# Kernel optimization log

Hardware: AMD Instinct MI355X
Metric: run time of the kernel (lower is better)

## Reference

```python
import jax, jax.numpy as jnp
import numpy as np

NEG_SLOPE = 0.2
EPS = 1e-16


def _gat_conv(x, edge_index, W, att_src, att_dst, bias):
    """PyG-style GATConv: linear -> per-edge attention -> segment softmax over dst -> scatter-sum.
    x: [N, Fin], W: [Fin, H*F], att_src/att_dst: [H, F], bias: [H*F].
    Adds self-loops (PyG default)."""
    N = x.shape[0]
    H, F = att_src.shape
    h = (x @ W).reshape(N, H, F)                       # [N, H, F]
    loops = jnp.arange(N, dtype=edge_index.dtype)
    src = jnp.concatenate([edge_index[0], loops])      # [E+N]
    dst = jnp.concatenate([edge_index[1], loops])
    a_s = jnp.sum(h * att_src[None], axis=-1)          # [N, H]
    a_d = jnp.sum(h * att_dst[None], axis=-1)          # [N, H]
    e = a_s[src] + a_d[dst]                            # [E+N, H]
    e = jnp.where(e > 0, e, NEG_SLOPE * e)             # leaky_relu
    m = jax.ops.segment_max(e, dst, num_segments=N)    # stable segment softmax
    ex = jnp.exp(e - m[dst])
    s = jax.ops.segment_sum(ex, dst, num_segments=N)
    alpha = ex / (s[dst] + EPS)                        # [E+N, H]
    msg = h[src] * alpha[..., None]                    # [E+N, H, F]
    out = jax.ops.segment_sum(msg, dst, num_segments=N)  # [N, H, F]
    return out.reshape(N, H * F) + bias


def setup_inputs() -> dict:
    key = jax.random.key(0)
    ks = jax.random.split(key, 12)
    N, E, Q = 200000, 6400000, 1000000
    return {
        "x": jax.random.normal(ks[0], (N, 1), jnp.float32),
        "edge_index": jax.random.randint(ks[1], (2, E), 0, N, jnp.int64),
        "src": jax.random.randint(ks[2], (Q,), 0, N, jnp.int64),
        "dst": jax.random.randint(ks[3], (Q,), 0, N, jnp.int64),
        "W1": jax.random.normal(ks[4], (1, 8), jnp.float32) * 0.5,
        "att_src1": jax.random.normal(ks[5], (2, 4), jnp.float32) * 0.5,
        "att_dst1": jax.random.normal(ks[6], (2, 4), jnp.float32) * 0.5,
        "b1": jnp.zeros((8,), jnp.float32),
        "W2": jax.random.normal(ks[7], (8, 8), jnp.float32) * 0.35,
        "att_src2": jax.random.normal(ks[8], (2, 4), jnp.float32) * 0.5,
        "att_dst2": jax.random.normal(ks[9], (2, 4), jnp.float32) * 0.5,
        "b2": jnp.zeros((8,), jnp.float32),
        "Wl": jax.random.normal(ks[10], (16, 2), jnp.float32) * 0.25,
        "bl": jnp.zeros((2,), jnp.float32),
    }


def reference(x, edge_index, src, dst, W1, att_src1, att_dst1, b1,
              W2, att_src2, att_dst2, b2, Wl, bl):
    h = _gat_conv(x, edge_index, W1, att_src1, att_dst1, b1)   # [N, 8]
    h = _gat_conv(h, edge_index, W2, att_src2, att_dst2, b2)   # [N, 8]
    y = jnp.concatenate([h[src], h[dst]], axis=-1)             # [Q, 16]
    return y @ Wl + bl                                         # [Q, 2]
```

## Files before the change

kernel.cpp:

```cpp
#include <hip/hip_runtime.h>
#include <hip/hip_fp16.h>

#define NEG_SLOPE 0.2f
#define GAT_EPS 1e-16f

#define BSHIFT 9
#define BSIZE 512
#define NBPAD 512
#define CAP_BKT 17664

#define K3_T 512
#define K3_VPT 16
#define K3_TILE (K3_T * K3_VPT)

#define CAP_BUILD 18432

#define LPD 16

typedef _Float16 half8 __attribute__((ext_vector_type(8)));

static __device__ __forceinline__ float leaky(float v) {
    return v > 0.0f ? v : NEG_SLOPE * v;
}


__global__ __launch_bounds__(K3_T) void bin_scatter_kernel(
        const int* __restrict__ src, const int* __restrict__ dst, int E, int NB,
        int* __restrict__ bcursor, unsigned int* __restrict__ binned) {
    extern __shared__ unsigned long long sbuf[];
    __shared__ int cnt[NBPAD];
    __shared__ int lstart[NBPAD];
    __shared__ int gbase[NBPAD];
    const int tid = threadIdx.x;
    const int t0 = blockIdx.x * K3_TILE;
    const int base = t0 + tid * K3_VPT;

    cnt[tid] = 0;
    __syncthreads();

    int b[K3_VPT];
    unsigned int v[K3_VPT];
    #pragma unroll
    for (int g = 0; g < K3_VPT / 4; ++g) {
        int off = base + g * 4;
        if (off < E) {
            int4 s4 = *(const int4*)(src + off);
            int4 d4 = *(const int4*)(dst + off);
            int ss[4] = {s4.x, s4.y, s4.z, s4.w};
            int dd[4] = {d4.x, d4.y, d4.z, d4.w};
            #pragma unroll
            for (int j = 0; j < 4; ++j) {
                int k = g * 4 + j;
                b[k] = dd[j] >> BSHIFT;
                v[k] = ((unsigned int)ss[j] << BSHIFT) | (unsigned int)(dd[j] & (BSIZE - 1));
                atomicAdd(&cnt[b[k]], 1);
            }
        } else {
            #pragma unroll
            for (int j = 0; j < 4; ++j) b[g * 4 + j] = -1;
        }
    }
    __syncthreads();

    int c = cnt[tid];
    lstart[tid] = c;
    __syncthreads();
    for (int ofs = 1; ofs < NBPAD; ofs <<= 1) {
        int t = (tid >= ofs) ? lstart[tid - ofs] : 0;
        __syncthreads();
        lstart[tid] += t;
        __syncthreads();
    }
    int excl = lstart[tid] - c;
    if (tid < NB) gbase[tid] = tid * CAP_BKT + (c ? atomicAdd(&bcursor[tid], c) : 0);
    __syncthreads();
    lstart[tid] = excl;
    cnt[tid] = 0;
    __syncthreads();

    #pragma unroll
    for (int k = 0; k < K3_VPT; ++k) {
        if (b[k] >= 0) {
            int r = atomicAdd(&cnt[b[k]], 1);
            int slot = lstart[b[k]] + r;
            sbuf[slot] = ((unsigned long long)(unsigned int)b[k] << 32) | v[k];
        }
    }
    __syncthreads();

    int nvalid = min(K3_TILE, E - t0);
    for (int j = tid; j < nvalid; j += K3_T) {
        unsigned long long p = sbuf[j];
        int bb = (int)(p >> 32);
        binned[gbase[bb] + (j - lstart[bb])] = (unsigned int)p;
    }
}


__global__ __launch_bounds__(BSIZE) void bucket_build_kernel(
        unsigned int* __restrict__ binned,
        const int* __restrict__ bcursor,
        int N,
        int2* __restrict__ rowrange) {
    extern __shared__ unsigned int sbuf32[];
    __shared__ int cnt[BSIZE];
    __shared__ int lstart[BSIZE];
    const int b = blockIdx.x;
    const int tid = threadIdx.x;
    const int e0 = b * CAP_BKT;
    const int nE = bcursor[b];
    const int n0 = b << BSHIFT;

    cnt[tid] = 0;
    __syncthreads();
    for (int i = tid; i < nE; i += BSIZE)
        atomicAdd(&cnt[binned[e0 + i] & (BSIZE - 1)], 1);
    __syncthreads();

    int c = cnt[tid];
    lstart[tid] = c;
    __syncthreads();
    for (int ofs = 1; ofs < BSIZE; ofs <<= 1) {
        int t = (tid >= ofs) ? lstart[tid - ofs] : 0;
        __syncthreads();
        lstart[tid] += t;
        __syncthreads();
    }
    int excl = lstart[tid] - c;
    __syncthreads();
    lstart[tid] = excl;
    cnt[tid] = 0;
    __syncthreads();

    int n = n0 + tid;
    if (n < N) rowrange[n] = make_int2(e0 + excl, e0 + excl + c);

    for (int i = tid; i < nE; i += BSIZE) {
        unsigned int v = binned[e0 + i];
        int dl = v & (BSIZE - 1);
        int r = atomicAdd(&cnt[dl], 1);
        int slot = lstart[dl] + r;
        if (slot < CAP_BUILD) sbuf32[slot] = v >> BSHIFT;
    }
    __syncthreads();

    int lim = min(nE, CAP_BUILD);
    for (int j = tid; j < lim; j += BSIZE)
        binned[e0 + j] = sbuf32[j];
}


__global__ void prep1_kernel(const float* __restrict__ x,
                             const float* __restrict__ W1,
                             const float* __restrict__ adw,
                             int N,
                             float2* __restrict__ adst,
                             half8* __restrict__ h16) {
    int n = blockIdx.x * blockDim.x + threadIdx.x;
    if (n >= N) return;
    float xv = x[n];
    float hv[8];
    #pragma unroll
    for (int j = 0; j < 8; ++j) hv[j] = xv * W1[j];
    float d0 = 0.f, d1 = 0.f;
    #pragma unroll
    for (int f = 0; f < 4; ++f) {
        d0 += hv[f] * adw[f];
        d1 += hv[4 + f] * adw[4 + f];
    }
    adst[n] = make_float2(d0, d1);
    half8 ho;
    #pragma unroll
    for (int j = 0; j < 8; ++j) ho[j] = (_Float16)hv[j];
    h16[n] = ho;
}


__global__ void prep2_kernel(const float* __restrict__ in,
                             const float* __restrict__ W2,
                             const float* __restrict__ adw,
                             int N,
                             float2* __restrict__ adst,
                             half8* __restrict__ h16) {
    int n = blockIdx.x * blockDim.x + threadIdx.x;
    if (n >= N) return;
    const float4* ip = (const float4*)(in + (size_t)n * 8);
    float4 i0 = ip[0], i1 = ip[1];
    float iv[8] = {i0.x, i0.y, i0.z, i0.w, i1.x, i1.y, i1.z, i1.w};
    float hv[8];
    #pragma unroll
    for (int j = 0; j < 8; ++j) {
        float acc = 0.f;
        #pragma unroll
        for (int k = 0; k < 8; ++k) acc += iv[k] * W2[k * 8 + j];
        hv[j] = acc;
    }
    float d0 = 0.f, d1 = 0.f;
    #pragma unroll
    for (int f = 0; f < 4; ++f) {
        d0 += hv[f] * adw[f];
        d1 += hv[4 + f] * adw[4 + f];
    }
    adst[n] = make_float2(d0, d1);
    half8 ho;
    #pragma unroll
    for (int j = 0; j < 8; ++j) ho[j] = (_Float16)hv[j];
    h16[n] = ho;
}


__global__ void gat_pass_kernel(const float2* __restrict__ adst,
                                const half8* __restrict__ h16,
                                const int2* __restrict__ rowrange,
                                const unsigned int* __restrict__ col,
                                const float* __restrict__ asw,
                                const float* __restrict__ bias,
                                int N,
                                float* __restrict__ out32,
                                half8* __restrict__ out16) {
    int t = blockIdx.x * blockDim.x + threadIdx.x;
    int n = t / LPD;
    int lane = t & (LPD - 1);
    if (n >= N) return;
    float w0 = asw[0], w1 = asw[1], w2 = asw[2], w3 = asw[3];
    float w4 = asw[4], w5 = asw[5], w6 = asw[6], w7 = asw[7];
    float2 ad = adst[n];
    float sum0 = 0.f, sum1 = 0.f;
    float acc[8] = {0.f, 0.f, 0.f, 0.f, 0.f, 0.f, 0.f, 0.f};
    if (lane == 0) {
        half8 hh = h16[n];
        float hs[8];
        #pragma unroll
        for (int k = 0; k < 8; ++k) hs[k] = (float)hh[k];
        float a0 = hs[0] * w0 + hs[1] * w1 + hs[2] * w2 + hs[3] * w3;
        float a1 = hs[4] * w4 + hs[5] * w5 + hs[6] * w6 + hs[7] * w7;
        float p0 = __expf(leaky(a0 + ad.x));
        float p1 = __expf(leaky(a1 + ad.y));
        sum0 = p0; sum1 = p1;
        #pragma unroll
        for (int k = 0; k < 4; ++k) { acc[k] = hs[k] * p0; acc[4 + k] = hs[4 + k] * p1; }
    }
    int2 rr = rowrange[n];
    int i = rr.x + lane;
    unsigned int s = (i < rr.y) ? __builtin_nontemporal_load(&col[i]) : 0u;
    while (i < rr.y) {
        int inext = i + LPD;
        unsigned int snext = (inext < rr.y) ? __builtin_nontemporal_load(&col[inext]) : 0u;
        half8 hh = h16[s];
        float hs[8];
        #pragma unroll
        for (int k = 0; k < 8; ++k) hs[k] = (float)hh[k];
        float a0 = hs[0] * w0 + hs[1] * w1 + hs[2] * w2 + hs[3] * w3;
        float a1 = hs[4] * w4 + hs[5] * w5 + hs[6] * w6 + hs[7] * w7;
        float q0 = __expf(leaky(a0 + ad.x));
        float q1 = __expf(leaky(a1 + ad.y));
        sum0 += q0; sum1 += q1;
        #pragma unroll
        for (int k = 0; k < 4; ++k) { acc[k] += hs[k] * q0; acc[4 + k] += hs[4 + k] * q1; }
        i = inext; s = snext;
    }
    #pragma unroll
    for (int ofs = 1; ofs < LPD; ofs <<= 1) {
        sum0 += __shfl_xor(sum0, ofs, LPD);
        sum1 += __shfl_xor(sum1, ofs, LPD);
        #pragma unroll
        for (int k = 0; k < 8; ++k) acc[k] += __shfl_xor(acc[k], ofs, LPD);
    }
    if (lane == 0) {
        float inv0 = 1.0f / (sum0 + GAT_EPS);
        float inv1 = 1.0f / (sum1 + GAT_EPS);
        float r[8];
        #pragma unroll
        for (int k = 0; k < 4; ++k) {
            r[k] = acc[k] * inv0 + bias[k];
            r[4 + k] = acc[4 + k] * inv1 + bias[4 + k];
        }
        if (out32) {
            float4* op = (float4*)(out32 + (size_t)n * 8);
            op[0] = make_float4(r[0], r[1], r[2], r[3]);
            op[1] = make_float4(r[4], r[5], r[6], r[7]);
        }
        if (out16) {
            half8 ho;
            #pragma unroll
            for (int k = 0; k < 8; ++k) ho[k] = (_Float16)r[k];
            out16[n] = ho;
        }
    }
}


__global__ void final_kernel(const half8* __restrict__ h2,
                             const int* __restrict__ srcq,
                             const int* __restrict__ dstq,
                             const float* __restrict__ Wl,
                             const float* __restrict__ bl,
                             int Q,
                             float* __restrict__ y) {
    int q = blockIdx.x * blockDim.x + threadIdx.x;
    if (q >= Q) return;
    int s = srcq[q];
    int d = dstq[q];
    half8 hs8 = h2[s];
    half8 hd8 = h2[d];
    float y0 = bl[0], y1 = bl[1];
    #pragma unroll
    for (int k = 0; k < 8; ++k) {
        float hv = (float)hs8[k];
        y0 += hv * Wl[k * 2 + 0];
        y1 += hv * Wl[k * 2 + 1];
    }
    #pragma unroll
    for (int k = 0; k < 8; ++k) {
        float hv = (float)hd8[k];
        y0 += hv * Wl[(8 + k) * 2 + 0];
        y1 += hv * Wl[(8 + k) * 2 + 1];
    }
    *(float2*)(y + (size_t)q * 2) = make_float2(y0, y1);
}


static inline size_t align_up(size_t v, size_t a) { return (v + a - 1) & ~(a - 1); }

extern "C" void kernel_launch(void* const* d_in, const int* in_sizes, int n_in,
                              void* d_out, int out_size, void* d_ws, size_t ws_size,
                              hipStream_t stream) {
    const float* x    = (const float*)d_in[0];
    const int*   ei   = (const int*)d_in[1];
    const int*   srcq = (const int*)d_in[2];
    const int*   dstq = (const int*)d_in[3];
    const float* W1   = (const float*)d_in[4];
    const float* as1  = (const float*)d_in[5];
    const float* ad1  = (const float*)d_in[6];
    const float* b1   = (const float*)d_in[7];
    const float* W2   = (const float*)d_in[8];
    const float* as2  = (const float*)d_in[9];
    const float* ad2  = (const float*)d_in[10];
    const float* b2   = (const float*)d_in[11];
    const float* Wl   = (const float*)d_in[12];
    const float* bl   = (const float*)d_in[13];

    const int N = in_sizes[0];
    const int E = in_sizes[1] / 2;
    const int Q = in_sizes[2];
    const int NB = (N + BSIZE - 1) >> BSHIFT;

    const int* esrc = ei;
    const int* edst = ei + E;

    char* w = (char*)d_ws;
    unsigned int* binned = (unsigned int*)w;  w += align_up((size_t)NB * CAP_BKT * 4, 256);
    int*    bcursor  = (int*)w;               w += align_up((size_t)NBPAD * 4, 256);
    int2*   rowrange = (int2*)w;              w += align_up((size_t)N * 8, 256);
    half8*  h16  = (half8*)w;                 w += align_up((size_t)N * 16, 256);
    float2* adst = (float2*)w;                w += align_up((size_t)N * 8, 256);
    float*  out1 = (float*)w;                 w += align_up((size_t)N * 8 * 4, 256);
    half8*  out2h = (half8*)w;

    const int BT = 256;
    int nodeBlocks = (N + BT - 1) / BT;
    int gatBlocks  = ((N * LPD) + BT - 1) / BT;
    int qBlocks    = (Q + BT - 1) / BT;
    int k3Blocks   = (E + K3_TILE - 1) / K3_TILE;

    hipMemsetAsync(bcursor, 0, (size_t)NBPAD * 4, stream);
    bin_scatter_kernel<<<k3Blocks, K3_T, (size_t)K3_TILE * 8, stream>>>(
        esrc, edst, E, NB, bcursor, binned);
    bucket_build_kernel<<<NB, BSIZE, (size_t)CAP_BUILD * 4, stream>>>(
        binned, bcursor, N, rowrange);

    prep1_kernel<<<nodeBlocks, BT, 0, stream>>>(x, W1, ad1, N, adst, h16);
    gat_pass_kernel<<<gatBlocks, BT, 0, stream>>>(adst, h16, rowrange, binned, as1, b1, N,
                                                  out1, (half8*)nullptr);

    prep2_kernel<<<nodeBlocks, BT, 0, stream>>>(out1, W2, ad2, N, adst, h16);
    gat_pass_kernel<<<gatBlocks, BT, 0, stream>>>(adst, h16, rowrange, binned, as2, b2, N,
                                                  (float*)nullptr, out2h);

    final_kernel<<<qBlocks, BT, 0, stream>>>(out2h, srcq, dstq, Wl, bl, Q, (float*)d_out);
}
```

Baseline: 185.3 us.

## Fuse layer-2 projection into GAT pass epilogue, unroll edge loop, retune sizes

Removes prep2_kernel by computing the W2 projection and destination attention inside the first GAT pass epilogue, writing fp16 features and adst into separate buffers. This drops the fp32 out1 round trip and one kernel launch. The edge loop now handles two edges per iteration to raise memory-level parallelism. Lanes per destination drop from 16 to 8 and bin-scatter items per thread rise from 16 to 32, with a scalar tail path for partial int4 groups.

```diff
diff --git a/kernel.cpp b/kernel.cpp
--- a/kernel.cpp
+++ b/kernel.cpp
@@ -10,12 +10,12 @@
 #define CAP_BKT 17664
 
 #define K3_T 512
-#define K3_VPT 16
+#define K3_VPT 32
 #define K3_TILE (K3_T * K3_VPT)
 
 #define CAP_BUILD 18432
 
-#define LPD 16
+#define LPD 8
 
 typedef _Float16 half8 __attribute__((ext_vector_type(8)));
 
@@ -43,7 +43,7 @@
     #pragma unroll
     for (int g = 0; g < K3_VPT / 4; ++g) {
         int off = base + g * 4;
-        if (off < E) {
+        if (off + 3 < E) {
             int4 s4 = *(const int4*)(src + off);
             int4 d4 = *(const int4*)(dst + off);
             int ss[4] = {s4.x, s4.y, s4.z, s4.w};
@@ -57,7 +57,17 @@
             }
         } else {
             #pragma unroll
-            for (int j = 0; j < 4; ++j) b[g * 4 + j] = -1;
+            for (int j = 0; j < 4; ++j) {
+                int k = g * 4 + j;
+                int i = off + j;
+                b[k] = -1;
+                if (i < E) {
+                    int d = dst[i];
+                    b[k] = d >> BSHIFT;
+                    v[k] = ((unsigned int)src[i] << BSHIFT) | (unsigned int)(d & (BSIZE - 1));
+                    atomicAdd(&cnt[b[k]], 1);
+                }
+            }
         }
     }
     __syncthreads();
@@ -176,39 +186,6 @@
 }
 
 
-__global__ void prep2_kernel(const float* __restrict__ in,
-                             const float* __restrict__ W2,
-                             const float* __restrict__ adw,
-                             int N,
-                             float2* __restrict__ adst,
-                             half8* __restrict__ h16) {
-    int n = blockIdx.x * blockDim.x + threadIdx.x;
-    if (n >= N) return;
-    const float4* ip = (const float4*)(in + (size_t)n * 8);
-    float4 i0 = ip[0], i1 = ip[1];
-    float iv[8] = {i0.x, i0.y, i0.z, i0.w, i1.x, i1.y, i1.z, i1.w};
-    float hv[8];
-    #pragma unroll
-    for (int j = 0; j < 8; ++j) {
-        float acc = 0.f;
-        #pragma unroll
-        for (int k = 0; k < 8; ++k) acc += iv[k] * W2[k * 8 + j];
-        hv[j] = acc;
-    }
-    float d0 = 0.f, d1 = 0.f;
-    #pragma unroll
-    for (int f = 0; f < 4; ++f) {
-        d0 += hv[f] * adw[f];
-        d1 += hv[4 + f] * adw[4 + f];
-    }
-    adst[n] = make_float2(d0, d1);
-    half8 ho;
-    #pragma unroll
-    for (int j = 0; j < 8; ++j) ho[j] = (_Float16)hv[j];
-    h16[n] = ho;
-}
-
-
 __global__ void gat_pass_kernel(const float2* __restrict__ adst,
                                 const half8* __restrict__ h16,
                                 const int2* __restrict__ rowrange,
@@ -216,8 +193,10 @@
                                 const float* __restrict__ asw,
                                 const float* __restrict__ bias,
                                 int N,
-                                float* __restrict__ out32,
-                                half8* __restrict__ out16) {
+                                const float* __restrict__ W2,
+                                const float* __restrict__ adw2,
+                                float2* __restrict__ adst2,
+                                half8* __restrict__ h16out) {
     int t = blockIdx.x * blockDim.x + threadIdx.x;
     int n = t / LPD;
     int lane = t & (LPD - 1);
@@ -240,25 +219,42 @@
         #pragma unroll
         for (int k = 0; k < 4; ++k) { acc[k] = hs[k] * p0; acc[4 + k] = hs[4 + k] * p1; }
     }
+
+#define GAT_PROC(hh)                                                            \
+    {                                                                           \
+        float hs[8];                                                            \
+        _Pragma("unroll")                                                       \
+        for (int k = 0; k < 8; ++k) hs[k] = (float)(hh)[k];                     \
+        float a0 = hs[0] * w0 + hs[1] * w1 + hs[2] * w2 + hs[3] * w3;           \
+        float a1 = hs[4] * w4 + hs[5] * w5 + hs[6] * w6 + hs[7] * w7;           \
+        float q0 = __expf(leaky(a0 + ad.x));                                    \
+        float q1 = __expf(leaky(a1 + ad.y));                                    \
+        sum0 += q0; sum1 += q1;                                                 \
+        _Pragma("unroll")                                                       \
+        for (int k = 0; k < 4; ++k) {                                           \
+            acc[k] += hs[k] * q0;                                               \
+            acc[4 + k] += hs[4 + k] * q1;                                       \
+        }                                                                       \
+    }
+
     int2 rr = rowrange[n];
     int i = rr.x + lane;
-    unsigned int s = (i < rr.y) ? __builtin_nontemporal_load(&col[i]) : 0u;
-    while (i < rr.y) {
-        int inext = i + LPD;
-        unsigned int snext = (inext < rr.y) ? __builtin_nontemporal_load(&col[inext]) : 0u;
+    while (i + LPD < rr.y) {
+        unsigned int sA = __builtin_nontemporal_load(&col[i]);
+        unsigned int sB = __builtin_nontemporal_load(&col[i + LPD]);
+        half8 hA = h16[sA];
+        half8 hB = h16[sB];
+        GAT_PROC(hA);
+        GAT_PROC(hB);
+        i += 2 * LPD;
+    }
+    if (i < rr.y) {
+        unsigned int s = __builtin_nontemporal_load(&col[i]);
         half8 hh = h16[s];
-        float hs[8];
-        #pragma unroll
-        for (int k = 0; k < 8; ++k) hs[k] = (float)hh[k];
-        float a0 = hs[0] * w0 + hs[1] * w1 + hs[2] * w2 + hs[3] * w3;
-        float a1 = hs[4] * w4 + hs[5] * w5 + hs[6] * w6 + hs[7] * w7;
-        float q0 = __expf(leaky(a0 + ad.x));
-        float q1 = __expf(leaky(a1 + ad.y));
-        sum0 += q0; sum1 += q1;
-        #pragma unroll
-        for (int k = 0; k < 4; ++k) { acc[k] += hs[k] * q0; acc[4 + k] += hs[4 + k] * q1; }
-        i = inext; s = snext;
-    }
+        GAT_PROC(hh);
+    }
+#undef GAT_PROC
+
     #pragma unroll
     for (int ofs = 1; ofs < LPD; ofs <<= 1) {
         sum0 += __shfl_xor(sum0, ofs, LPD);
@@ -275,16 +271,31 @@
             r[k] = acc[k] * inv0 + bias[k];
             r[4 + k] = acc[4 + k] * inv1 + bias[4 + k];
         }
-        if (out32) {
-            float4* op = (float4*)(out32 + (size_t)n * 8);
-            op[0] = make_float4(r[0], r[1], r[2], r[3]);
-            op[1] = make_float4(r[4], r[5], r[6], r[7]);
-        }
-        if (out16) {
+        if (W2) {
+            float hv[8];
+            #pragma unroll
+            for (int j = 0; j < 8; ++j) {
+                float s = 0.f;
+                #pragma unroll
+                for (int k = 0; k < 8; ++k) s += r[k] * W2[k * 8 + j];
+                hv[j] = s;
+            }
+            float d0 = 0.f, d1 = 0.f;
+            #pragma unroll
+            for (int f = 0; f < 4; ++f) {
+                d0 += hv[f] * adw2[f];
+                d1 += hv[4 + f] * adw2[4 + f];
+            }
+            adst2[n] = make_float2(d0, d1);
             half8 ho;
             #pragma unroll
+            for (int k = 0; k < 8; ++k) ho[k] = (_Float16)hv[k];
+            h16out[n] = ho;
+        } else {
+            half8 ho;
+            #pragma unroll
             for (int k = 0; k < 8; ++k) ho[k] = (_Float16)r[k];
-            out16[n] = ho;
+            h16out[n] = ho;
         }
     }
 }
@@ -352,9 +363,10 @@
     unsigned int* binned = (unsigned int*)w;  w += align_up((size_t)NB * CAP_BKT * 4, 256);
     int*    bcursor  = (int*)w;               w += align_up((size_t)NBPAD * 4, 256);
     int2*   rowrange = (int2*)w;              w += align_up((size_t)N * 8, 256);
-    half8*  h16  = (half8*)w;                 w += align_up((size_t)N * 16, 256);
-    float2* adst = (float2*)w;                w += align_up((size_t)N * 8, 256);
-    float*  out1 = (float*)w;                 w += align_up((size_t)N * 8 * 4, 256);
+    half8*  h16a  = (half8*)w;                w += align_up((size_t)N * 16, 256);
+    float2* adsta = (float2*)w;               w += align_up((size_t)N * 8, 256);
+    half8*  h16b  = (half8*)w;                w += align_up((size_t)N * 16, 256);
+    float2* adstb = (float2*)w;               w += align_up((size_t)N * 8, 256);
     half8*  out2h = (half8*)w;
 
     const int BT = 256;
@@ -369,13 +381,13 @@
     bucket_build_kernel<<<NB, BSIZE, (size_t)CAP_BUILD * 4, stream>>>(
         binned, bcursor, N, rowrange);
 
-    prep1_kernel<<<nodeBlocks, BT, 0, stream>>>(x, W1, ad1, N, adst, h16);
-    gat_pass_kernel<<<gatBlocks, BT, 0, stream>>>(adst, h16, rowrange, binned, as1, b1, N,
-                                                  out1, (half8*)nullptr);
-
-    prep2_kernel<<<nodeBlocks, BT, 0, stream>>>(out1, W2, ad2, N, adst, h16);
-    gat_pass_kernel<<<gatBlocks, BT, 0, stream>>>(adst, h16, rowrange, binned, as2, b2, N,
-                                                  (float*)nullptr, out2h);
+    prep1_kernel<<<nodeBlocks, BT, 0, stream>>>(x, W1, ad1, N, adsta, h16a);
+    gat_pass_kernel<<<gatBlocks, BT, 0, stream>>>(adsta, h16a, rowrange, binned, as1, b1, N,
+                                                  W2, ad2, adstb, h16b);
+
+    gat_pass_kernel<<<gatBlocks, BT, 0, stream>>>(adstb, h16b, rowrange, binned, as2, b2, N,
+                                                  (const float*)nullptr, (const float*)nullptr,
+                                                  (float2*)nullptr, out2h);
 
     final_kernel<<<qBlocks, BT, 0, stream>>>(out2h, srcq, dstq, Wl, bl, Q, (float*)d_out);
 }
```

After: 199.4 us. 1.08x slower.
